# Performance work log

Hardware: AMD Instinct MI355X
Metric: run time of the kernel (lower is better)

## Reference

```python
import jax, jax.numpy as jnp
import numpy as np

B, M, D, DE = 2, 256, 256, 64  # batch, tokens, in_dim, dep_embed_dim


def setup_inputs() -> dict:
    key = jax.random.key(0)
    ks = jax.random.split(key, 10)
    features = jax.random.normal(ks[0], (B, M + 1, D), jnp.float32)
    dep_type_adj = jax.random.normal(ks[1], (B, M, M, DE), jnp.float32)
    adj = (jax.random.uniform(ks[2], (B, M, M)) < 0.05).astype(jnp.int32)
    idx = jnp.arange(M)
    adj = adj.at[:, idx, idx].set(1)
    asp_start = jax.random.randint(ks[3], (B,), 0, 200, dtype=jnp.int32)
    asp_end = asp_start + 16
    s = lambda fan_in: 1.0 / np.sqrt(fan_in)
    Wz = jax.random.normal(ks[4], (D, D), jnp.float32) * s(D)
    bz = jax.random.normal(ks[5], (D,), jnp.float32) * s(D)
    Wa = jax.random.normal(ks[6], (D + DE + D,), jnp.float32) * s(D + DE + D)
    Wm = jax.random.normal(ks[7], (D, D + DE), jnp.float32) * s(D + DE)
    Wh = jax.random.normal(ks[8], (D, 2 * D), jnp.float32) * s(2 * D)
    return dict(features=features, dep_type_adj=dep_type_adj, deprel_adj=adj,
                asp_start=asp_start, asp_end=asp_end,
                Wz=Wz, bz=bz, Wa=Wa, Wm=Wm, Wh=Wh)


def reference(features, dep_type_adj, deprel_adj, asp_start, asp_end, Wz, bz, Wa, Wm, Wh):
    # z_linear
    zf = features @ Wz.T + bz                              # [B, M+1, D]
    f = zf[:, 1:]                                          # token feats [B, M, D]
    asp = zf[0, 1:]                                        # NOTE: original indexes features[0] (batch 0)

    # candidate neighbors for node i: out-edges (i,j) then in-edges (j,i) -> 2M slots
    dep_cat = jnp.concatenate([dep_type_adj, jnp.swapaxes(dep_type_adj, 1, 2)], axis=2)  # [B,M,2M,DE]
    mask = jnp.concatenate([deprel_adj, jnp.swapaxes(deprel_adj, 1, 2)], axis=2) != 0    # [B,M,2M]

    # attention_layer weight split over [dep | neighbor_feat | aspect_feat]
    wa_dep, wa_nf, wa_asp = Wa[:DE], Wa[DE:DE + D], Wa[DE + D:]
    s = (jnp.einsum('bike,e->bik', dep_cat, wa_dep)
         + jnp.tile(f @ wa_nf, (1, 2))[:, None, :]
         + (asp @ wa_asp)[None, :, None])                  # [B,M,2M]
    s = jnp.where(s > 0, s, 0.01 * s)                      # LeakyReLU(0.01)
    big_neg = jnp.finfo(s.dtype).min
    w = jax.nn.softmax(jnp.where(mask, s, big_neg), axis=-1)
    w = jnp.where(mask, w, 0.0)                            # edge-softmax over valid neighbors

    # w_m over [dep | neighbor_feat]
    Wm_dep, Wm_f = Wm[:, :DE], Wm[:, DE:]
    nf_proj = jnp.tile(f @ Wm_f.T, (1, 2, 1))              # [B,2M,D], neighbor part (i-independent)
    msg = jax.nn.relu(jnp.einsum('bike,de->bikd', dep_cat, Wm_dep) + nf_proj[:, None])  # [B,M,2M,D]
    fused = jnp.einsum('bik,bikd->bid', w, msg)            # weighted aggregate [B,M,D]

    # w_h over [fused | aspect]
    out_asp = jax.nn.relu(fused @ Wh[:, :D].T + (asp @ Wh[:, D:].T)[None])  # [B,M,D]

    # only aspect-span nodes are updated; +1 offset into the token axis
    pos = jnp.arange(M)
    upd = (pos[None, :] >= asp_start[:, None]) & (pos[None, :] < asp_end[:, None])  # [B,M]
    tokens = jnp.where(upd[..., None], out_asp, features[:, 1:])
    return jnp.concatenate([features[:, :1], tokens], axis=1)  # dropout is identity at inference
```

## Files before the change

### kernel.cpp

```cpp
#include <hip/hip_runtime.h>
#include <hip/hip_bf16.h>
#include <cstdint>

#define BB 2
#define MM 256
#define DD 256
#define DE 64
#define K2 (2*MM)
#define WM_LD (DD+DE)
#define WH_LD (2*DD)
#define TM 8

__device__ float g_fproj[BB*MM*DD];
__device__ float g_asph [MM*DD];
__device__ float g_fnf  [BB*MM];
__device__ float g_aspdot[MM];

__global__ __launch_bounds__(256) void k_copy(const float4* __restrict__ src,
                                              float4* __restrict__ dst, int n4) {
  int i = blockIdx.x * 256 + threadIdx.x;
  if (i < n4) dst[i] = src[i];
}

__global__ __launch_bounds__(256) void k_pre(const float* __restrict__ feats,
                                             const float* __restrict__ Wz,
                                             const float* __restrict__ bz,
                                             const float* __restrict__ Wa,
                                             const float* __restrict__ Wm,
                                             const float* __restrict__ Wh) {
  const int blk = blockIdx.x;
  const int b   = (blk * TM) / MM;
  const int m0  = (blk * TM) % MM;
  const int d   = threadIdx.x;

  __shared__ float fin[TM][DD];
  __shared__ float fz [TM][DD];

  #pragma unroll
  for (int r = 0; r < TM; ++r)
    fin[r][d] = feats[((size_t)b*(MM+1) + m0 + r + 1)*DD + d];
  __syncthreads();

  float acc[TM];
  #pragma unroll
  for (int r = 0; r < TM; ++r) acc[r] = 0.f;
  {
    const float4* wrow = (const float4*)(Wz + (size_t)d * DD);
    for (int e4 = 0; e4 < DD/4; ++e4) {
      float4 w4 = wrow[e4];
      #pragma unroll
      for (int r = 0; r < TM; ++r) {
        const float* fp = &fin[r][e4*4];
        acc[r] += w4.x*fp[0] + w4.y*fp[1] + w4.z*fp[2] + w4.w*fp[3];
      }
    }
  }
  const float bzd = bz[d];
  #pragma unroll
  for (int r = 0; r < TM; ++r) { acc[r] += bzd; fz[r][d] = acc[r]; }
  __syncthreads();

  const int wv = d >> 6, lane = d & 63;
  for (int r = wv; r < TM; r += 4) {
    float p = 0.f;
    for (int e = lane; e < DD; e += 64) p += fz[r][e] * Wa[DE + e];
    for (int off = 32; off > 0; off >>= 1) p += __shfl_down(p, off, 64);
    if (lane == 0) g_fnf[b*MM + m0 + r] = p;
  }
  if (b == 0) {
    for (int r = wv; r < TM; r += 4) {
      float p = 0.f;
      for (int e = lane; e < DD; e += 64) p += fz[r][e] * Wa[DE + DD + e];
      for (int off = 32; off > 0; off >>= 1) p += __shfl_down(p, off, 64);
      if (lane == 0) g_aspdot[m0 + r] = p;
    }
  }

  #pragma unroll
  for (int r = 0; r < TM; ++r) acc[r] = 0.f;
  {
    const float4* wrow = (const float4*)(Wm + (size_t)d * WM_LD + DE);
    for (int e4 = 0; e4 < DD/4; ++e4) {
      float4 w4 = wrow[e4];
      #pragma unroll
      for (int r = 0; r < TM; ++r) {
        const float* fp = &fz[r][e4*4];
        acc[r] += w4.x*fp[0] + w4.y*fp[1] + w4.z*fp[2] + w4.w*fp[3];
      }
    }
  }
  #pragma unroll
  for (int r = 0; r < TM; ++r) g_fproj[((size_t)b*MM + m0 + r)*DD + d] = acc[r];

  if (b == 0) {
    #pragma unroll
    for (int r = 0; r < TM; ++r) acc[r] = 0.f;
    const float4* wrow = (const float4*)(Wh + (size_t)d * WH_LD + DD);
    for (int e4 = 0; e4 < DD/4; ++e4) {
      float4 w4 = wrow[e4];
      #pragma unroll
      for (int r = 0; r < TM; ++r) {
        const float* fp = &fz[r][e4*4];
        acc[r] += w4.x*fp[0] + w4.y*fp[1] + w4.z*fp[2] + w4.w*fp[3];
      }
    }
    #pragma unroll
    for (int r = 0; r < TM; ++r) g_asph[(size_t)(m0 + r)*DD + d] = acc[r];
  }
}

__global__ __launch_bounds__(256) void k_attn(const float* __restrict__ dta,
                                              const int*   __restrict__ adj,
                                              const int*   __restrict__ a_start,
                                              const int*   __restrict__ a_end,
                                              const float* __restrict__ Wa,
                                              const float* __restrict__ Wm,
                                              const float* __restrict__ Wh,
                                              float* __restrict__ out) {
  const int b = blockIdx.x >> 4;
  const int r = blockIdx.x & 15;
  const int i = a_start[b] + r;
  if (i >= a_end[b] || i >= MM) return;
  const int t = threadIdx.x;

  __shared__ int   act[K2];
  __shared__ float sv [K2];
  __shared__ float red[256];
  __shared__ int   wcnt[4];
  __shared__ float wadep[DE];
  __shared__ float depsh[64*DE];
  __shared__ float fused_sh[DD];

  if (t < DE) wadep[t] = Wa[t];

  const int lane = t & 63, wv = t >> 6;
  int na = 0;
  for (int phase = 0; phase < 2; ++phase) {
    const int k = phase*256 + t;
    const int mval = (k < MM) ? adj[((size_t)b*MM + i)*MM + k]
                              : adj[((size_t)b*MM + (k - MM))*MM + i];
    const bool on = (mval != 0);
    const unsigned long long bal = __ballot(on);
    if (lane == 0) wcnt[wv] = __popcll(bal);
    __syncthreads();
    int off = na;
    for (int w2 = 0; w2 < wv; ++w2) off += wcnt[w2];
    off += __popcll(bal & ((1ull << lane) - 1ull));
    if (on) act[off] = k;
    na += wcnt[0] + wcnt[1] + wcnt[2] + wcnt[3];
    __syncthreads();
  }

  const float aspdot_i = g_aspdot[i];
  for (int j = t; j < na; j += 256) {
    const int k = act[j];
    const float* dv = (k < MM) ? dta + (((size_t)b*MM + i)*MM + k)*DE
                               : dta + (((size_t)b*MM + (k - MM))*MM + i)*DE;
    float s = 0.f;
    const float4* dv4 = (const float4*)dv;
    #pragma unroll
    for (int e4 = 0; e4 < DE/4; ++e4) {
      const float4 v = dv4[e4];
      s += v.x*wadep[4*e4] + v.y*wadep[4*e4+1] + v.z*wadep[4*e4+2] + v.w*wadep[4*e4+3];
    }
    s += g_fnf[b*MM + (k & (MM-1))] + aspdot_i;
    sv[j] = (s > 0.f) ? s : 0.01f * s;
  }
  __syncthreads();

  float part = -3.4e38f;
  for (int j = t; j < na; j += 256) part = fmaxf(part, sv[j]);
  red[t] = part; __syncthreads();
  for (int s = 128; s > 0; s >>= 1) { if (t < s) red[t] = fmaxf(red[t], red[t+s]); __syncthreads(); }
  const float mx = red[0];
  __syncthreads();
  float psum = 0.f;
  for (int j = t; j < na; j += 256) { float e = expf(sv[j] - mx); sv[j] = e; psum += e; }
  red[t] = psum; __syncthreads();
  for (int s = 128; s > 0; s >>= 1) { if (t < s) red[t] += red[t+s]; __syncthreads(); }
  const float inv = 1.f / red[0];
  __syncthreads();
  for (int j = t; j < na; j += 256) sv[j] *= inv;
  __syncthreads();

  const int d = t;
  float wm[DE];
  {
    const float4* wmrow = (const float4*)(Wm + (size_t)d * WM_LD);
    #pragma unroll
    for (int e4 = 0; e4 < DE/4; ++e4) {
      float4 v = wmrow[e4];
      wm[4*e4] = v.x; wm[4*e4+1] = v.y; wm[4*e4+2] = v.z; wm[4*e4+3] = v.w;
    }
  }
  float acc = 0.f;
  for (int base = 0; base < na; base += 64) {
    const int cnt = min(64, na - base);
    const int nf4 = cnt * (DE/4);
    for (int q = t; q < nf4; q += 256) {
      const int jl = q >> 4, e4 = q & 15;
      const int k = act[base + jl];
      const float* dv = (k < MM) ? dta + (((size_t)b*MM + i)*MM + k)*DE
                                 : dta + (((size_t)b*MM + (k - MM))*MM + i)*DE;
      ((float4*)(depsh + jl*DE))[e4] = ((const float4*)dv)[e4];
    }
    __syncthreads();
    for (int jl = 0; jl < cnt; ++jl) {
      const int k = act[base + jl];
      const float* dp = depsh + jl*DE;
      float dot = 0.f;
      #pragma unroll
      for (int e4 = 0; e4 < DE/4; ++e4) {
        const float4 v = *(const float4*)(dp + 4*e4);
        dot += v.x*wm[4*e4] + v.y*wm[4*e4+1] + v.z*wm[4*e4+2] + v.w*wm[4*e4+3];
      }
      float msg = dot + g_fproj[((size_t)b*MM + (k & (MM-1)))*DD + d];
      msg = (msg > 0.f) ? msg : 0.f;
      acc += sv[base + jl] * msg;
    }
    __syncthreads();
  }
  fused_sh[d] = acc;
  __syncthreads();

  const float4* whrow = (const float4*)(Wh + (size_t)d * WH_LD);
  float o = 0.f;
  for (int e4 = 0; e4 < DD/4; ++e4) {
    float4 v = whrow[e4];
    const float* fp = &fused_sh[e4*4];
    o += v.x*fp[0] + v.y*fp[1] + v.z*fp[2] + v.w*fp[3];
  }
  o += g_asph[(size_t)i*DD + d];
  out[((size_t)b*(MM+1) + i + 1)*DD + d] = (o > 0.f) ? o : 0.f;
}

extern "C" void kernel_launch(void* const* d_in, const int* in_sizes, int n_in,
                              void* d_out, int out_size, void* d_ws, size_t ws_size,
                              hipStream_t stream) {
  const float* feats   = (const float*)d_in[0];
  const float* dta     = (const float*)d_in[1];
  const int*   adj     = (const int*)  d_in[2];
  const int*   a_start = (const int*)  d_in[3];
  const int*   a_end   = (const int*)  d_in[4];
  const float* Wz      = (const float*)d_in[5];
  const float* bz      = (const float*)d_in[6];
  const float* Wa      = (const float*)d_in[7];
  const float* Wm      = (const float*)d_in[8];
  const float* Wh      = (const float*)d_in[9];
  float* out = (float*)d_out;

  const int n4 = BB*(MM+1)*DD/4;
  k_copy<<<(n4 + 255)/256, 256, 0, stream>>>((const float4*)feats, (float4*)out, n4);
  k_pre <<<BB*MM/TM, 256, 0, stream>>>(feats, Wz, bz, Wa, Wm, Wh);
  k_attn<<<BB*16, 256, 0, stream>>>(dta, adj, a_start, a_end, Wa, Wm, Wh, out);
}
```

Measured before the change: 151.1 us.

## Transpose weights for coalesced projection and move aspect projection into attention kernel

Adds a pre-kernel that transposes Wz and the neighbor slice of Wm into global scratch, fused with the feature copy into the output. The projection kernel now handles two rows per block over more blocks and reads the transposed weights with coalesced per-thread loads. The aspect dot product and the aspect half of the Wh projection are no longer precomputed for all tokens; they are computed only for the 16 span rows inside the attention kernel from a stored batch-0 z vector. This aims to improve memory coalescing and parallelism in the precompute stage and drop work for tokens that are never updated. The cost is an extra transpose pass on every call and a bit more per-block work in the attention kernel.

```diff
diff --git a/kernel.cpp b/kernel.cpp
--- a/kernel.cpp
+++ b/kernel.cpp
@@ -9,104 +9,84 @@
 #define K2 (2*MM)
 #define WM_LD (DD+DE)
 #define WH_LD (2*DD)
-#define TM 8
-
+
+__device__ float g_fz   [MM*DD];
 __device__ float g_fproj[BB*MM*DD];
-__device__ float g_asph [MM*DD];
 __device__ float g_fnf  [BB*MM];
-__device__ float g_aspdot[MM];
-
-__global__ __launch_bounds__(256) void k_copy(const float4* __restrict__ src,
-                                              float4* __restrict__ dst, int n4) {
-  int i = blockIdx.x * 256 + threadIdx.x;
-  if (i < n4) dst[i] = src[i];
+__device__ float g_WzT  [DD*DD];
+__device__ float g_WmT  [DD*DD];
+
+__global__ __launch_bounds__(256) void k_tr(const float* __restrict__ Wz,
+                                            const float* __restrict__ Wm,
+                                            const float4* __restrict__ src,
+                                            float4* __restrict__ dst, int n4) {
+  const int t = threadIdx.x;
+  const int blk = blockIdx.x;
+  const int d = blk & 255;
+  if (blk < 256) g_WzT[t*DD + d] = Wz[(size_t)d*DD + t];
+  else           g_WmT[t*DD + d] = Wm[(size_t)d*WM_LD + DE + t];
+  const int idx = blk*256 + t;
+  if (idx < n4) dst[idx] = src[idx];
 }
 
 __global__ __launch_bounds__(256) void k_pre(const float* __restrict__ feats,
-                                             const float* __restrict__ Wz,
                                              const float* __restrict__ bz,
-                                             const float* __restrict__ Wa,
-                                             const float* __restrict__ Wm,
-                                             const float* __restrict__ Wh) {
+                                             const float* __restrict__ Wa) {
   const int blk = blockIdx.x;
-  const int b   = (blk * TM) / MM;
-  const int m0  = (blk * TM) % MM;
-  const int d   = threadIdx.x;
-
-  __shared__ float fin[TM][DD];
-  __shared__ float fz [TM][DD];
-
-  #pragma unroll
-  for (int r = 0; r < TM; ++r)
-    fin[r][d] = feats[((size_t)b*(MM+1) + m0 + r + 1)*DD + d];
-  __syncthreads();
-
-  float acc[TM];
-  #pragma unroll
-  for (int r = 0; r < TM; ++r) acc[r] = 0.f;
-  {
-    const float4* wrow = (const float4*)(Wz + (size_t)d * DD);
-    for (int e4 = 0; e4 < DD/4; ++e4) {
-      float4 w4 = wrow[e4];
-      #pragma unroll
-      for (int r = 0; r < TM; ++r) {
-        const float* fp = &fin[r][e4*4];
-        acc[r] += w4.x*fp[0] + w4.y*fp[1] + w4.z*fp[2] + w4.w*fp[3];
-      }
-    }
-  }
-  const float bzd = bz[d];
-  #pragma unroll
-  for (int r = 0; r < TM; ++r) { acc[r] += bzd; fz[r][d] = acc[r]; }
-  __syncthreads();
-
-  const int wv = d >> 6, lane = d & 63;
-  for (int r = wv; r < TM; r += 4) {
+  const int b   = blk >> 7;
+  const int m0  = (blk & 127) * 2;
+  const int t   = threadIdx.x;
+
+  __shared__ float fin[2][DD];
+  __shared__ float fzsh[2][DD];
+
+  fin[0][t] = feats[((size_t)b*(MM+1) + m0 + 1)*DD + t];
+  fin[1][t] = feats[((size_t)b*(MM+1) + m0 + 2)*DD + t];
+  __syncthreads();
+
+  float a0 = 0.f, a1 = 0.f;
+  #pragma unroll 8
+  for (int e4 = 0; e4 < DD/4; ++e4) {
+    const float4 f0 = *(const float4*)&fin[0][e4*4];
+    const float4 f1 = *(const float4*)&fin[1][e4*4];
+    const float w0 = g_WzT[(e4*4+0)*DD + t];
+    const float w1 = g_WzT[(e4*4+1)*DD + t];
+    const float w2 = g_WzT[(e4*4+2)*DD + t];
+    const float w3 = g_WzT[(e4*4+3)*DD + t];
+    a0 += f0.x*w0 + f0.y*w1 + f0.z*w2 + f0.w*w3;
+    a1 += f1.x*w0 + f1.y*w1 + f1.z*w2 + f1.w*w3;
+  }
+  const float bzt = bz[t];
+  a0 += bzt; a1 += bzt;
+  fzsh[0][t] = a0; fzsh[1][t] = a1;
+  if (b == 0) {
+    g_fz[(size_t)(m0    )*DD + t] = a0;
+    g_fz[(size_t)(m0 + 1)*DD + t] = a1;
+  }
+  __syncthreads();
+
+  const int wv = t >> 6, lane = t & 63;
+  if (wv < 2) {
     float p = 0.f;
-    for (int e = lane; e < DD; e += 64) p += fz[r][e] * Wa[DE + e];
+    for (int e = lane; e < DD; e += 64) p += fzsh[wv][e] * Wa[DE + e];
     for (int off = 32; off > 0; off >>= 1) p += __shfl_down(p, off, 64);
-    if (lane == 0) g_fnf[b*MM + m0 + r] = p;
-  }
-  if (b == 0) {
-    for (int r = wv; r < TM; r += 4) {
-      float p = 0.f;
-      for (int e = lane; e < DD; e += 64) p += fz[r][e] * Wa[DE + DD + e];
-      for (int off = 32; off > 0; off >>= 1) p += __shfl_down(p, off, 64);
-      if (lane == 0) g_aspdot[m0 + r] = p;
-    }
-  }
-
-  #pragma unroll
-  for (int r = 0; r < TM; ++r) acc[r] = 0.f;
-  {
-    const float4* wrow = (const float4*)(Wm + (size_t)d * WM_LD + DE);
-    for (int e4 = 0; e4 < DD/4; ++e4) {
-      float4 w4 = wrow[e4];
-      #pragma unroll
-      for (int r = 0; r < TM; ++r) {
-        const float* fp = &fz[r][e4*4];
-        acc[r] += w4.x*fp[0] + w4.y*fp[1] + w4.z*fp[2] + w4.w*fp[3];
-      }
-    }
-  }
-  #pragma unroll
-  for (int r = 0; r < TM; ++r) g_fproj[((size_t)b*MM + m0 + r)*DD + d] = acc[r];
-
-  if (b == 0) {
-    #pragma unroll
-    for (int r = 0; r < TM; ++r) acc[r] = 0.f;
-    const float4* wrow = (const float4*)(Wh + (size_t)d * WH_LD + DD);
-    for (int e4 = 0; e4 < DD/4; ++e4) {
-      float4 w4 = wrow[e4];
-      #pragma unroll
-      for (int r = 0; r < TM; ++r) {
-        const float* fp = &fz[r][e4*4];
-        acc[r] += w4.x*fp[0] + w4.y*fp[1] + w4.z*fp[2] + w4.w*fp[3];
-      }
-    }
-    #pragma unroll
-    for (int r = 0; r < TM; ++r) g_asph[(size_t)(m0 + r)*DD + d] = acc[r];
-  }
+    if (lane == 0) g_fnf[b*MM + m0 + wv] = p;
+  }
+
+  float p0 = 0.f, p1 = 0.f;
+  #pragma unroll 8
+  for (int e4 = 0; e4 < DD/4; ++e4) {
+    const float4 f0 = *(const float4*)&fzsh[0][e4*4];
+    const float4 f1 = *(const float4*)&fzsh[1][e4*4];
+    const float w0 = g_WmT[(e4*4+0)*DD + t];
+    const float w1 = g_WmT[(e4*4+1)*DD + t];
+    const float w2 = g_WmT[(e4*4+2)*DD + t];
+    const float w3 = g_WmT[(e4*4+3)*DD + t];
+    p0 += f0.x*w0 + f0.y*w1 + f0.z*w2 + f0.w*w3;
+    p1 += f1.x*w0 + f1.y*w1 + f1.z*w2 + f1.w*w3;
+  }
+  g_fproj[((size_t)b*MM + m0    )*DD + t] = p0;
+  g_fproj[((size_t)b*MM + m0 + 1)*DD + t] = p1;
 }
 
 __global__ __launch_bounds__(256) void k_attn(const float* __restrict__ dta,
@@ -128,10 +108,21 @@
   __shared__ float red[256];
   __shared__ int   wcnt[4];
   __shared__ float wadep[DE];
+  __shared__ float fz0[DD];
   __shared__ float depsh[64*DE];
   __shared__ float fused_sh[DD];
+  __shared__ float aspd_sh;
 
   if (t < DE) wadep[t] = Wa[t];
+  fz0[t] = g_fz[(size_t)i*DD + t];
+  __syncthreads();
+
+  red[t] = fz0[t] * Wa[DE + DD + t];
+  __syncthreads();
+  for (int s = 128; s > 0; s >>= 1) { if (t < s) red[t] += red[t+s]; __syncthreads(); }
+  if (t == 0) aspd_sh = red[0];
+  __syncthreads();
+  const float aspdot_i = aspd_sh;
 
   const int lane = t & 63, wv = t >> 6;
   int na = 0;
@@ -151,7 +142,6 @@
     __syncthreads();
   }
 
-  const float aspdot_i = g_aspdot[i];
   for (int j = t; j < na; j += 256) {
     const int k = act[j];
     const float* dv = (k < MM) ? dta + (((size_t)b*MM + i)*MM + k)*DE
@@ -206,7 +196,6 @@
     }
     __syncthreads();
     for (int jl = 0; jl < cnt; ++jl) {
-      const int k = act[base + jl];
       const float* dp = depsh + jl*DE;
       float dot = 0.f;
       #pragma unroll
@@ -214,6 +203,7 @@
         const float4 v = *(const float4*)(dp + 4*e4);
         dot += v.x*wm[4*e4] + v.y*wm[4*e4+1] + v.z*wm[4*e4+2] + v.w*wm[4*e4+3];
       }
+      const int k = act[base + jl];
       float msg = dot + g_fproj[((size_t)b*MM + (k & (MM-1)))*DD + d];
       msg = (msg > 0.f) ? msg : 0.f;
       acc += sv[base + jl] * msg;
@@ -225,12 +215,18 @@
 
   const float4* whrow = (const float4*)(Wh + (size_t)d * WH_LD);
   float o = 0.f;
-  for (int e4 = 0; e4 < DD/4; ++e4) {
-    float4 v = whrow[e4];
+  #pragma unroll 4
+  for (int e4 = 0; e4 < DD/4; ++e4) {
+    const float4 v = whrow[e4];
     const float* fp = &fused_sh[e4*4];
     o += v.x*fp[0] + v.y*fp[1] + v.z*fp[2] + v.w*fp[3];
   }
-  o += g_asph[(size_t)i*DD + d];
+  #pragma unroll 4
+  for (int e4 = 0; e4 < DD/4; ++e4) {
+    const float4 v = whrow[DD/4 + e4];
+    const float* fp = &fz0[e4*4];
+    o += v.x*fp[0] + v.y*fp[1] + v.z*fp[2] + v.w*fp[3];
+  }
   out[((size_t)b*(MM+1) + i + 1)*DD + d] = (o > 0.f) ? o : 0.f;
 }
 
@@ -250,7 +246,7 @@
   float* out = (float*)d_out;
 
   const int n4 = BB*(MM+1)*DD/4;
-  k_copy<<<(n4 + 255)/256, 256, 0, stream>>>((const float4*)feats, (float4*)out, n4);
-  k_pre <<<BB*MM/TM, 256, 0, stream>>>(feats, Wz, bz, Wa, Wm, Wh);
+  k_tr  <<<2*DD, 256, 0, stream>>>(Wz, Wm, (const float4*)feats, (float4*)out, n4);
+  k_pre <<<BB*MM/2, 256, 0, stream>>>(feats, bz, Wa);
   k_attn<<<BB*16, 256, 0, stream>>>(dta, adj, a_start, a_end, Wa, Wm, Wh, out);
 }
```

Result: no change. 148.3 us (-1.8%).
